# Kernel tuning notes

Measured on AMD Instinct MI355X. Metric: run time of the kernel, lower is better.

Reference implementation:

```python
import jax, jax.numpy as jnp
import numpy as np

SPARSITY = 0.01

def quantize(weight, s):
    # ternary quantization: (-s, 0, +s); computed under no_grad in torch
    pos = (weight > s).astype(weight.dtype)
    neg = (weight < -s).astype(weight.dtype)
    return (pos - neg) * s

def setup_inputs() -> dict:
    key = jax.random.key(0)
    k1, k2, k3 = jax.random.split(key, 3)
    B, N, Din, Dout = 8, 2048, 256, 256
    x = jax.random.normal(k1, (B, N, Din), dtype=jnp.float32)
    adj = jax.random.uniform(k2, (B, N, N), dtype=jnp.float32)
    # xavier_uniform_ over (in_dim, out_dim)
    limit = float(np.sqrt(6.0 / (Din + Dout)))
    weight = jax.random.uniform(k3, (Din, Dout), dtype=jnp.float32, minval=-limit, maxval=limit)
    bias = jnp.zeros((Dout,), dtype=jnp.float32)
    return {"x": x, "adj": adj, "weight": weight, "bias": bias}

def reference(x, adj, weight, bias):
    dw = quantize(weight, SPARSITY)          # [Din, Dout] ternary * s
    support = jnp.einsum('bni,io->bno', x, dw)   # [B, N, Dout]
    out = jnp.einsum('bnm,bmo->bno', adj, support) + bias
    return jax.nn.relu(out)
```

## Files before the change

kernel.cpp:

```cpp
#include <hip/hip_runtime.h>
#include <stdint.h>

typedef __attribute__((ext_vector_type(8))) short short8;
typedef __attribute__((ext_vector_type(4))) float f32x4;

static_assert(sizeof(short8) == 16, "frag size");

__device__ __forceinline__ uint16_t f2bf(float f) {
  uint32_t u = __builtin_bit_cast(uint32_t, f);
  u += 0x7fffu + ((u >> 16) & 1u);
  return (uint16_t)(u >> 16);
}

__device__ __forceinline__ short8 pack_bf16x8(f32x4 lo, f32x4 hi) {
  union { uint32_t u[4]; short8 s; } z;
  z.u[0] = (uint32_t)f2bf(lo.x) | ((uint32_t)f2bf(lo.y) << 16);
  z.u[1] = (uint32_t)f2bf(lo.z) | ((uint32_t)f2bf(lo.w) << 16);
  z.u[2] = (uint32_t)f2bf(hi.x) | ((uint32_t)f2bf(hi.y) << 16);
  z.u[3] = (uint32_t)f2bf(hi.z) | ((uint32_t)f2bf(hi.w) << 16);
  return z.s;
}

__device__ __forceinline__ void gload_lds16(const void* g, void* lds_wave_base) {
  __builtin_amdgcn_global_load_lds(
      (__attribute__((address_space(1))) void*)(void*)(g),
      (__attribute__((address_space(3))) void*)(lds_wave_base),
      16, 0, 0);
}

#define MEMFENCE() asm volatile("" ::: "memory")

__global__ __launch_bounds__(256) void quant_kernel(const float* __restrict__ w,
                                                    uint16_t* __restrict__ dwT) {
  const int o = blockIdx.x, i = threadIdx.x;
  const float v = w[i * 256 + o];
  const float t = (v > 0.01f) ? 1.0f : ((v < -0.01f) ? -1.0f : 0.0f);
  dwT[o * 256 + (i ^ ((o & 7) << 3))] = f2bf(t);
}

#define SB_A 0
#define SB_B 32768

__global__ __launch_bounds__(256) void support_kernel(const float* __restrict__ x,
                                                      const uint16_t* __restrict__ dwT,
                                                      uint16_t* __restrict__ spt) {
  __shared__ __align__(16) unsigned char smem[65536];
  const int t = threadIdx.x, lane = t & 63, w = t >> 6;
  const int r = lane & 15, q = lane >> 4;
  const int g0 = (blockIdx.x & 255) * 64;
  const int o0 = (blockIdx.x >> 8) * 64;

#pragma unroll
  for (int j = 0; j < 8; ++j) {
    const int id = j * 256 + t;
    const int row = id >> 5, c = id & 31;
    const float* p = x + (size_t)(g0 + row) * 256 + c * 8;
    const f32x4 v0 = *(const f32x4*)p;
    const f32x4 v1 = *(const f32x4*)(p + 4);
    uint4 u;
    u.x = (uint32_t)f2bf(v0.x) | ((uint32_t)f2bf(v0.y) << 16);
    u.y = (uint32_t)f2bf(v0.z) | ((uint32_t)f2bf(v0.w) << 16);
    u.z = (uint32_t)f2bf(v1.x) | ((uint32_t)f2bf(v1.y) << 16);
    u.w = (uint32_t)f2bf(v1.z) | ((uint32_t)f2bf(v1.w) << 16);
    *(uint4*)(smem + SB_A + row * 512 + ((c ^ (row & 7)) << 4)) = u;
  }
#pragma unroll
  for (int j = 0; j < 8; ++j) {
    const int id = j * 256 + t, row = id >> 5, c = id & 31;
    gload_lds16(dwT + (size_t)(o0 + row) * 256 + c * 8,
                smem + SB_B + (size_t)(j * 256 + w * 64) * 16);
  }
  __syncthreads();

  f32x4 acc[4] = {};
#pragma unroll
  for (int h = 0; h < 8; ++h) {
    short8 av, bv[4];
    const int pc = (((h * 4 + q) ^ (r & 7)) << 4);
    av = *(const short8*)(smem + SB_A + (16 * w + r) * 512 + pc);
#pragma unroll
    for (int ni = 0; ni < 4; ++ni)
      bv[ni] = *(const short8*)(smem + SB_B + (16 * ni + r) * 512 + pc);
#pragma unroll
    for (int ni = 0; ni < 4; ++ni)
      acc[ni] = __builtin_amdgcn_mfma_f32_16x16x32_bf16(av, bv[ni], acc[ni], 0, 0, 0);
  }
  __syncthreads();

#pragma unroll
  for (int ni = 0; ni < 4; ++ni) {
    const int ol = 16 * ni + r;
#pragma unroll
    for (int reg = 0; reg < 4; ++reg) {
      const int gl = 16 * w + 4 * q + reg;
      const int gsw = gl ^ ((ol & 7) << 3);
      *(uint16_t*)(smem + (ol * 64 + gsw) * 2) = f2bf(acc[ni][reg] * 0.01f);
    }
  }
  __syncthreads();
#pragma unroll
  for (int it = 0; it < 2; ++it) {
    const int id = it * 256 + t, row = id >> 3, cc = id & 7;
    const uint4 u = *(const uint4*)(smem + (row * 64 + cc * 8) * 2);
    *(uint4*)(spt + (size_t)(o0 + row) * 16384 + g0 + cc * 8) = u;
  }
}

#define MBUF0 0u
#define MBUF1 49152u
#define MBUF2 98304u
#define MB_BOFF 16384u

__global__ __launch_bounds__(512, 2) void gcn_main_kernel(const float* __restrict__ adj,
                                                          const uint16_t* __restrict__ spt,
                                                          const float* __restrict__ bias,
                                                          float* __restrict__ out) {
  __shared__ __align__(16) unsigned char smem[147456];
  const int t = threadIdx.x, lane = t & 63, wv = t >> 6;
  const int r = lane & 15, q = lane >> 4;
  const int wn = wv >> 2;
  const int oq = wv & 3;
  const int bb = blockIdx.x & 7;
  const int n0 = (blockIdx.x >> 3) * 64;
  const float* adjb = adj + ((size_t)bb * 2048 + n0) * 2048;
  const uint16_t* sptb = spt + (size_t)bb * 2048;

  const int aRow0 = wv * 8 + (lane >> 4);
  const int aCl = lane & 15;
  const int aCs0 = (aCl & 8) | ((aCl & 7) ^ (aRow0 & 7));
  const int aCs1 = (aCl & 8) | ((aCl & 7) ^ ((aRow0 + 4) & 7));
  const float* aSrc0 = adjb + (size_t)aRow0 * 2048 + aCs0 * 4;
  const float* aSrc1 = adjb + (size_t)(aRow0 + 4) * 2048 + aCs1 * 4;
  const unsigned aDst0 = (unsigned)(wv * 2) * 1024u;
  const unsigned aDst1 = aDst0 + 1024u;

  const int bRowIn = lane >> 3, bCl = lane & 7;

#define STAGE(K0, BASE)                                                        \
  do {                                                                         \
    gload_lds16(aSrc0 + (K0), smem + (BASE) + aDst0);                          \
    gload_lds16(aSrc1 + (K0), smem + (BASE) + aDst1);                          \
    _Pragma("unroll") for (int j = 0; j < 4; ++j) {                            \
      const int row_ = (4 * wv + j) * 8 + bRowIn;                              \
      gload_lds16(sptb + (size_t)row_ * 16384 + (K0) + bCl * 8,                \
                  smem + (BASE) + MB_BOFF + (size_t)(4 * wv + j) * 1024);      \
    }                                                                          \
    MEMFENCE();                                                                \
  } while (0)

  f32x4 acc[2][4] = {};
  const int rr = r & 7;

  STAGE(0, MBUF0);
  STAGE(64, MBUF1);
  asm volatile("s_waitcnt vmcnt(6)" ::: "memory");
  __builtin_amdgcn_s_barrier();

  unsigned bufCur = MBUF0, bufNxt = MBUF1, bufNxt2 = MBUF2;

  for (int kt = 0; kt < 32; ++kt) {
    if (kt < 30) STAGE((kt + 2) * 64, bufNxt2);

#pragma unroll
    for (int h = 0; h < 2; ++h) {
      short8 av[2], bv[4];
#pragma unroll
      for (int mi = 0; mi < 2; ++mi) {
        const int row = wn * 32 + mi * 16 + r;
        const int g0 = h * 8 + 2 * q;
        const int c0 = (g0 & 8) | ((g0 & 7) ^ (row & 7));
        const int c1 = (g0 & 8) | (((g0 + 1) & 7) ^ (row & 7));
        const f32x4 a0 = *(const f32x4*)(smem + bufCur + row * 256 + c0 * 16);
        const f32x4 a1 = *(const f32x4*)(smem + bufCur + row * 256 + c1 * 16);
        av[mi] = pack_bf16x8(a0, a1);
      }
      const int pc = (((h * 4 + q) ^ rr) << 4);
#pragma unroll
      for (int ni = 0; ni < 4; ++ni)
        bv[ni] = *(const short8*)(smem + bufCur + MB_BOFF +
                                  (oq * 64 + 16 * ni + r) * 128 + pc);
#pragma unroll
      for (int mi = 0; mi < 2; ++mi)
#pragma unroll
        for (int ni = 0; ni < 4; ++ni)
          acc[mi][ni] = __builtin_amdgcn_mfma_f32_16x16x32_bf16(av[mi], bv[ni],
                                                                acc[mi][ni], 0, 0, 0);
    }

    if (kt < 31) {
      if (kt < 30) {
        asm volatile("s_waitcnt vmcnt(6)" ::: "memory");
      } else {
        asm volatile("s_waitcnt vmcnt(0)" ::: "memory");
      }
      __builtin_amdgcn_s_barrier();
      const unsigned tmp = bufCur; bufCur = bufNxt; bufNxt = bufNxt2; bufNxt2 = tmp;
    }
  }

#pragma unroll
  for (int ni = 0; ni < 4; ++ni) {
    const int o = oq * 64 + 16 * ni + r;
    const float bs = bias[o];
#pragma unroll
    for (int mi = 0; mi < 2; ++mi)
#pragma unroll
      for (int reg = 0; reg < 4; ++reg) {
        const int n = n0 + wn * 32 + mi * 16 + 4 * q + reg;
        out[((size_t)bb * 2048 + n) * 256 + o] = fmaxf(acc[mi][ni][reg] + bs, 0.0f);
      }
  }
#undef STAGE
}

extern "C" void kernel_launch(void* const* d_in, const int* in_sizes, int n_in,
                              void* d_out, int out_size, void* d_ws, size_t ws_size,
                              hipStream_t stream) {
  const float* x      = (const float*)d_in[0];
  const float* adj    = (const float*)d_in[1];
  const float* weight = (const float*)d_in[2];
  const float* bias   = (const float*)d_in[3];
  float* out = (float*)d_out;

  uint16_t* dwT = (uint16_t*)d_ws;
  uint16_t* spt = (uint16_t*)((char*)d_ws + 131072);

  hipLaunchKernelGGL(quant_kernel,    dim3(256),  dim3(256), 0, stream, weight, dwT);
  hipLaunchKernelGGL(support_kernel,  dim3(1024), dim3(256), 0, stream, x, dwT, spt);
  hipLaunchKernelGGL(gcn_main_kernel, dim3(256),  dim3(512), 0, stream, adj, spt, bias, out);
}
```

Baseline: 228.8 us.

## Pre-convert adjacency to bf16 and use 128x128 tiled bf16 main GEMM

Adds a separate kernel that converts the fp32 adjacency matrix to a pre-swizzled bf16 copy in workspace. A new main kernel then streams bf16 tiles of both operands straight into LDS with direct global-to-LDS loads, double-buffered, and computes 128x128 output tiles with MFMA. This removes the per-iteration fp32-to-bf16 packing from the hot loop. The cost is an extra full pass over adj plus a 64MB write, and adj being re-read once per output-column tile. The old path is kept as a fallback when the workspace is too small.

```diff
diff --git a/kernel.cpp b/kernel.cpp
--- a/kernel.cpp
+++ b/kernel.cpp
@@ -30,12 +30,33 @@
 
 #define MEMFENCE() asm volatile("" ::: "memory")
 
+
 __global__ __launch_bounds__(256) void quant_kernel(const float* __restrict__ w,
                                                     uint16_t* __restrict__ dwT) {
   const int o = blockIdx.x, i = threadIdx.x;
   const float v = w[i * 256 + o];
   const float t = (v > 0.01f) ? 1.0f : ((v < -0.01f) ? -1.0f : 0.0f);
   dwT[o * 256 + (i ^ ((o & 7) << 3))] = f2bf(t);
+}
+
+__global__ __launch_bounds__(256) void convA_kernel(const float* __restrict__ adj,
+                                                    uint16_t* __restrict__ adjbf) {
+#pragma unroll
+  for (int it = 0; it < 8; ++it) {
+    const int id = blockIdx.x * 2048 + it * 256 + threadIdx.x;
+    const int row = id >> 8;
+    const int c = id & 255;
+    const int srcc = (c & 248) | ((c & 7) ^ (row & 7));
+    const float* p = adj + (size_t)row * 2048 + srcc * 8;
+    const f32x4 v0 = *(const f32x4*)p;
+    const f32x4 v1 = *(const f32x4*)(p + 4);
+    uint4 u;
+    u.x = (uint32_t)f2bf(v0.x) | ((uint32_t)f2bf(v0.y) << 16);
+    u.y = (uint32_t)f2bf(v0.z) | ((uint32_t)f2bf(v0.w) << 16);
+    u.z = (uint32_t)f2bf(v1.x) | ((uint32_t)f2bf(v1.y) << 16);
+    u.w = (uint32_t)f2bf(v1.z) | ((uint32_t)f2bf(v1.w) << 16);
+    *(uint4*)(adjbf + (size_t)row * 2048 + c * 8) = u;
+  }
 }
 
 #define SB_A 0
@@ -106,15 +127,99 @@
   }
 }
 
+#define GA0 0u
+#define GB0 16384u
+#define GA1 32768u
+#define GB1 49152u
+
+__global__ __launch_bounds__(256, 2) void gcn_main_v9(const uint16_t* __restrict__ adjbf,
+                                                      const uint16_t* __restrict__ spt,
+                                                      const float* __restrict__ bias,
+                                                      float* __restrict__ out) {
+  __shared__ __align__(16) unsigned char smem[65536];
+  const int t = threadIdx.x, lane = t & 63, wv = t >> 6;
+  const int r = lane & 15, q = lane >> 4, rr = r & 7;
+  const int wn = wv >> 1, wo = wv & 1;
+  const int bb = blockIdx.x & 7;
+  const int nt = (blockIdx.x >> 3) & 15;
+  const int ot = blockIdx.x >> 7;
+  const int n0 = nt * 128, o0 = ot * 128;
+  const uint16_t* Ab = adjbf + ((size_t)bb * 2048 + n0) * 2048;
+  const uint16_t* Bb = spt + (size_t)bb * 2048;
+
+  const int dr = lane >> 3, dc = lane & 7;
+  const int rbase0 = (wv * 4) * 8 + dr;
+
+#define STAGE(K0, ABASE, BBASE)                                                \
+  do {                                                                         \
+    _Pragma("unroll") for (int j = 0; j < 4; ++j) {                            \
+      gload_lds16(Ab + (size_t)(rbase0 + j * 8) * 2048 + (K0) + dc * 8,        \
+                  smem + (ABASE) + (size_t)(wv * 4 + j) * 1024);               \
+    }                                                                          \
+    _Pragma("unroll") for (int j = 0; j < 4; ++j) {                            \
+      gload_lds16(Bb + (size_t)(o0 + rbase0 + j * 8) * 16384 + (K0) + dc * 8,  \
+                  smem + (BBASE) + (size_t)(wv * 4 + j) * 1024);               \
+    }                                                                          \
+    MEMFENCE();                                                                \
+  } while (0)
+
+  f32x4 acc[4][4] = {};
+
+  STAGE(0, GA0, GB0);
+  __syncthreads();
+
+  for (int kt = 0; kt < 32; ++kt) {
+    const unsigned aCur = (kt & 1) ? GA1 : GA0;
+    const unsigned bCur = (kt & 1) ? GB1 : GB0;
+    const unsigned aNxt = (kt & 1) ? GA0 : GA1;
+    const unsigned bNxt = (kt & 1) ? GB0 : GB1;
+
+    if (kt < 31) STAGE((kt + 1) * 64, aNxt, bNxt);
+
+#pragma unroll
+    for (int h = 0; h < 2; ++h) {
+      const int pc = (((h * 4 + q) ^ rr) << 4);
+      short8 av[4], bv[4];
+#pragma unroll
+      for (int mi = 0; mi < 4; ++mi)
+        av[mi] = *(const short8*)(smem + aCur + (wn * 64 + 16 * mi + r) * 128 + pc);
+#pragma unroll
+      for (int ni = 0; ni < 4; ++ni)
+        bv[ni] = *(const short8*)(smem + bCur + (wo * 64 + 16 * ni + r) * 128 + pc);
+#pragma unroll
+      for (int mi = 0; mi < 4; ++mi)
+#pragma unroll
+        for (int ni = 0; ni < 4; ++ni)
+          acc[mi][ni] = __builtin_amdgcn_mfma_f32_16x16x32_bf16(av[mi], bv[ni],
+                                                                acc[mi][ni], 0, 0, 0);
+    }
+    __syncthreads();
+  }
+
+#pragma unroll
+  for (int ni = 0; ni < 4; ++ni) {
+    const int o = o0 + wo * 64 + 16 * ni + r;
+    const float bs = bias[o];
+#pragma unroll
+    for (int mi = 0; mi < 4; ++mi)
+#pragma unroll
+      for (int reg = 0; reg < 4; ++reg) {
+        const int n = n0 + wn * 64 + 16 * mi + 4 * q + reg;
+        out[((size_t)bb * 2048 + n) * 256 + o] = fmaxf(acc[mi][ni][reg] + bs, 0.0f);
+      }
+  }
+#undef STAGE
+}
+
 #define MBUF0 0u
 #define MBUF1 49152u
 #define MBUF2 98304u
 #define MB_BOFF 16384u
 
-__global__ __launch_bounds__(512, 2) void gcn_main_kernel(const float* __restrict__ adj,
-                                                          const uint16_t* __restrict__ spt,
-                                                          const float* __restrict__ bias,
-                                                          float* __restrict__ out) {
+__global__ __launch_bounds__(512, 2) void gcn_main_v8(const float* __restrict__ adj,
+                                                      const uint16_t* __restrict__ spt,
+                                                      const float* __restrict__ bias,
+                                                      float* __restrict__ out) {
   __shared__ __align__(16) unsigned char smem[147456];
   const int t = threadIdx.x, lane = t & 63, wv = t >> 6;
   const int r = lane & 15, q = lane >> 4;
@@ -225,7 +330,15 @@
   uint16_t* dwT = (uint16_t*)d_ws;
   uint16_t* spt = (uint16_t*)((char*)d_ws + 131072);
 
-  hipLaunchKernelGGL(quant_kernel,    dim3(256),  dim3(256), 0, stream, weight, dwT);
-  hipLaunchKernelGGL(support_kernel,  dim3(1024), dim3(256), 0, stream, x, dwT, spt);
-  hipLaunchKernelGGL(gcn_main_kernel, dim3(256),  dim3(512), 0, stream, adj, spt, bias, out);
-}
+  hipLaunchKernelGGL(quant_kernel,   dim3(256),  dim3(256), 0, stream, weight, dwT);
+  hipLaunchKernelGGL(support_kernel, dim3(1024), dim3(256), 0, stream, x, dwT, spt);
+
+  const size_t NEED = 131072u + 8388608u + 67108864u;
+  if (ws_size >= NEED) {
+    uint16_t* adjbf = (uint16_t*)((char*)d_ws + 131072 + 8388608);
+    hipLaunchKernelGGL(convA_kernel, dim3(2048), dim3(256), 0, stream, adj, adjbf);
+    hipLaunchKernelGGL(gcn_main_v9,  dim3(256),  dim3(256), 0, stream, adjbf, spt, bias, out);
+  } else {
+    hipLaunchKernelGGL(gcn_main_v8,  dim3(256),  dim3(512), 0, stream, adj, spt, bias, out);
+  }
+}
```

After: 255.0 us. +11.4%, slower.

## Retile main GCN kernel to 128x128 output tiles with 256-thread blocks

Applied to the files above, without the earlier changes.

Changes the adjacency-times-support kernel from 64-row by full-256-column tiles with 8 waves to 128x128 tiles with 4 waves, each wave computing a 64x64 sub-tile. This raises MFMA work per loaded fragment and halves support traffic per block. In exchange, each adj row is now loaded and converted to bf16 by two blocks, doubling adj reads, and each CU runs fewer waves.

```diff
diff --git a/kernel.cpp b/kernel.cpp
--- a/kernel.cpp
+++ b/kernel.cpp
@@ -29,6 +29,7 @@
 }
 
 #define MEMFENCE() asm volatile("" ::: "memory")
+
 
 __global__ __launch_bounds__(256) void quant_kernel(const float* __restrict__ w,
                                                     uint16_t* __restrict__ dwT) {
@@ -106,70 +107,64 @@
   }
 }
 
-#define MBUF0 0u
-#define MBUF1 49152u
-#define MBUF2 98304u
-#define MB_BOFF 16384u
-
-__global__ __launch_bounds__(512, 2) void gcn_main_kernel(const float* __restrict__ adj,
-                                                          const uint16_t* __restrict__ spt,
-                                                          const float* __restrict__ bias,
-                                                          float* __restrict__ out) {
+#define VBUFSZ 49152u
+#define VB_B 32768u
+
+__global__ __launch_bounds__(256) void gcn_main_kernel(const float* __restrict__ adj,
+                                                       const uint16_t* __restrict__ spt,
+                                                       const float* __restrict__ bias,
+                                                       float* __restrict__ out) {
   __shared__ __align__(16) unsigned char smem[147456];
   const int t = threadIdx.x, lane = t & 63, wv = t >> 6;
-  const int r = lane & 15, q = lane >> 4;
-  const int wn = wv >> 2;
-  const int oq = wv & 3;
+  const int r = lane & 15, q = lane >> 4, rr = r & 7;
+  const int wn = wv >> 1, wo = wv & 1;
   const int bb = blockIdx.x & 7;
-  const int n0 = (blockIdx.x >> 3) * 64;
-  const float* adjb = adj + ((size_t)bb * 2048 + n0) * 2048;
-  const uint16_t* sptb = spt + (size_t)bb * 2048;
-
-  const int aRow0 = wv * 8 + (lane >> 4);
-  const int aCl = lane & 15;
-  const int aCs0 = (aCl & 8) | ((aCl & 7) ^ (aRow0 & 7));
-  const int aCs1 = (aCl & 8) | ((aCl & 7) ^ ((aRow0 + 4) & 7));
-  const float* aSrc0 = adjb + (size_t)aRow0 * 2048 + aCs0 * 4;
-  const float* aSrc1 = adjb + (size_t)(aRow0 + 4) * 2048 + aCs1 * 4;
-  const unsigned aDst0 = (unsigned)(wv * 2) * 1024u;
-  const unsigned aDst1 = aDst0 + 1024u;
-
-  const int bRowIn = lane >> 3, bCl = lane & 7;
+  const int nt = (blockIdx.x >> 3) & 15;
+  const int ot = blockIdx.x >> 7;
+  const int n0 = nt * 128, o0 = ot * 128;
+  const float* Ab = adj + ((size_t)bb * 2048 + n0) * 2048;
+  const uint16_t* Bb = spt + (size_t)bb * 2048;
+
+  const int aRowL = lane >> 4, aCl = lane & 15;
+  const int bRowL = lane >> 3, bCl = lane & 7;
 
 #define STAGE(K0, BASE)                                                        \
   do {                                                                         \
-    gload_lds16(aSrc0 + (K0), smem + (BASE) + aDst0);                          \
-    gload_lds16(aSrc1 + (K0), smem + (BASE) + aDst1);                          \
+    _Pragma("unroll") for (int j = 0; j < 8; ++j) {                            \
+      const int row_ = wv * 32 + j * 4 + aRowL;                                \
+      const int cs_ = (aCl & 8) | ((aCl & 7) ^ (row_ & 7));                    \
+      gload_lds16(Ab + (size_t)row_ * 2048 + (K0) + cs_ * 4,                   \
+                  smem + (BASE) + (size_t)(wv * 8 + j) * 1024);                \
+    }                                                                          \
     _Pragma("unroll") for (int j = 0; j < 4; ++j) {                            \
-      const int row_ = (4 * wv + j) * 8 + bRowIn;                              \
-      gload_lds16(sptb + (size_t)row_ * 16384 + (K0) + bCl * 8,                \
-                  smem + (BASE) + MB_BOFF + (size_t)(4 * wv + j) * 1024);      \
+      const int row_ = (wv * 4 + j) * 8 + bRowL;                               \
+      gload_lds16(Bb + (size_t)(o0 + row_) * 16384 + (K0) + bCl * 8,           \
+                  smem + (BASE) + VB_B + (size_t)(wv * 4 + j) * 1024);         \
     }                                                                          \
     MEMFENCE();                                                                \
   } while (0)
 
-  f32x4 acc[2][4] = {};
-  const int rr = r & 7;
-
-  STAGE(0, MBUF0);
-  STAGE(64, MBUF1);
-  asm volatile("s_waitcnt vmcnt(6)" ::: "memory");
+  f32x4 acc[4][4] = {};
+
+  STAGE(0, 0u);
+  STAGE(64, VBUFSZ);
+  asm volatile("s_waitcnt vmcnt(12)" ::: "memory");
   __builtin_amdgcn_s_barrier();
 
-  unsigned bufCur = MBUF0, bufNxt = MBUF1, bufNxt2 = MBUF2;
+  unsigned bufCur = 0u, bufNxt = VBUFSZ, bufNxt2 = 2u * VBUFSZ;
 
   for (int kt = 0; kt < 32; ++kt) {
     if (kt < 30) STAGE((kt + 2) * 64, bufNxt2);
 
 #pragma unroll
     for (int h = 0; h < 2; ++h) {
-      short8 av[2], bv[4];
-#pragma unroll
-      for (int mi = 0; mi < 2; ++mi) {
-        const int row = wn * 32 + mi * 16 + r;
-        const int g0 = h * 8 + 2 * q;
-        const int c0 = (g0 & 8) | ((g0 & 7) ^ (row & 7));
-        const int c1 = (g0 & 8) | (((g0 + 1) & 7) ^ (row & 7));
+      short8 av[4], bv[4];
+#pragma unroll
+      for (int mi = 0; mi < 4; ++mi) {
+        const int row = wn * 64 + 16 * mi + r;
+        const int g = h * 8 + 2 * q;
+        const int c0 = (g & 8) | ((g & 7) ^ rr);
+        const int c1 = (g & 8) | (((g + 1) & 7) ^ rr);
         const f32x4 a0 = *(const f32x4*)(smem + bufCur + row * 256 + c0 * 16);
         const f32x4 a1 = *(const f32x4*)(smem + bufCur + row * 256 + c1 * 16);
         av[mi] = pack_bf16x8(a0, a1);
@@ -177,10 +172,10 @@
       const int pc = (((h * 4 + q) ^ rr) << 4);
 #pragma unroll
       for (int ni = 0; ni < 4; ++ni)
-        bv[ni] = *(const short8*)(smem + bufCur + MB_BOFF +
-                                  (oq * 64 + 16 * ni + r) * 128 + pc);
-#pragma unroll
-      for (int mi = 0; mi < 2; ++mi)
+        bv[ni] = *(const short8*)(smem + bufCur + VB_B +
+                                  (wo * 64 + 16 * ni + r) * 128 + pc);
+#pragma unroll
+      for (int mi = 0; mi < 4; ++mi)
 #pragma unroll
         for (int ni = 0; ni < 4; ++ni)
           acc[mi][ni] = __builtin_amdgcn_mfma_f32_16x16x32_bf16(av[mi], bv[ni],
@@ -189,7 +184,7 @@
 
     if (kt < 31) {
       if (kt < 30) {
-        asm volatile("s_waitcnt vmcnt(6)" ::: "memory");
+        asm volatile("s_waitcnt vmcnt(12)" ::: "memory");
       } else {
         asm volatile("s_waitcnt vmcnt(0)" ::: "memory");
       }
@@ -200,13 +195,13 @@
 
 #pragma unroll
   for (int ni = 0; ni < 4; ++ni) {
-    const int o = oq * 64 + 16 * ni + r;
+    const int o = o0 + wo * 64 + 16 * ni + r;
     const float bs = bias[o];
 #pragma unroll
-    for (int mi = 0; mi < 2; ++mi)
+    for (int mi = 0; mi < 4; ++mi)
 #pragma unroll
       for (int reg = 0; reg < 4; ++reg) {
-        const int n = n0 + wn * 32 + mi * 16 + 4 * q + reg;
+        const int n = n0 + wn * 64 + 16 * mi + 4 * q + reg;
         out[((size_t)bb * 2048 + n) * 256 + o] = fmaxf(acc[mi][ni][reg] + bs, 0.0f);
       }
   }
@@ -227,5 +222,5 @@
 
   hipLaunchKernelGGL(quant_kernel,    dim3(256),  dim3(256), 0, stream, weight, dwT);
   hipLaunchKernelGGL(support_kernel,  dim3(1024), dim3(256), 0, stream, x, dwT, spt);
-  hipLaunchKernelGGL(gcn_main_kernel, dim3(256),  dim3(512), 0, stream, adj, spt, bias, out);
-}
+  hipLaunchKernelGGL(gcn_main_kernel, dim3(256),  dim3(256), 0, stream, adj, spt, bias, out);
+}
```

After: 229.7 us. Within noise of the previous version (+0.4%).
